# Kernel optimization log

Measured on AMD Instinct MI355X. Metric: run time of the kernel, lower is better.

## Reference

```python
import jax, jax.numpy as jnp
import numpy as np

# FCHL19 representation (Christensen et al., JCP 2020), as implemented by
# QMLightning's pairlist_gpu/egto_gpu/fchl_gpu CUDA kernels, re-expressed as
# dense masked pair/triplet tensors (non-periodic: cell/inv_cell empty).
SPECIES = np.array([1.0, 6.0, 7.0, 8.0], dtype=np.float32)
NSPEC = 4
NRS2 = 24
NRS3 = 20
RCUT = 8.0
ETA2 = 0.32
ETA3 = 2.7
TWO_BODY_DECAY = 1.8
THREE_BODY_DECAY = 0.57
THREE_BODY_WEIGHT = float(np.sqrt(ETA3 / np.pi) * 13.4)  # module pre-scales weight
RS2 = np.linspace(0.0, RCUT, NRS2 + 1)[1:].astype(np.float32)
RS3 = np.linspace(0.0, RCUT, NRS3 + 1)[1:].astype(np.float32)
NPAIR = NSPEC * (NSPEC + 1) // 2  # unordered species pairs -> 10

def _pair_map():
    M = np.zeros((NSPEC, NSPEC, NPAIR), np.float32)
    i = 0
    for p in range(NSPEC):
        for q in range(p, NSPEC):
            M[p, q, i] = 1.0
            M[q, p, i] = 1.0
            i += 1
    return M
PAIR_MAP = _pair_map()

B_MOL, MAX_ATOMS = 64, 28


def setup_inputs() -> dict:
    key = jax.random.key(0)
    k1, k2, k3 = jax.random.split(key, 3)
    X = jax.random.uniform(k1, (B_MOL, MAX_ATOMS, 3), jnp.float32) * 6.0
    atom_counts = jax.random.randint(k2, (B_MOL,), 24, MAX_ATOMS + 1).astype(jnp.int32)
    zidx = jax.random.randint(k3, (B_MOL, MAX_ATOMS), 0, NSPEC)
    valid = jnp.arange(MAX_ATOMS)[None, :] < atom_counts[:, None]
    Z = jnp.where(valid, jnp.asarray(SPECIES)[zidx], 0.0).astype(jnp.float32)
    atomIDs = jnp.arange(B_MOL * MAX_ATOMS, dtype=jnp.int32)
    molIDs = jnp.repeat(jnp.arange(B_MOL, dtype=jnp.int32), MAX_ATOMS)
    return {"X": X, "Z": Z, "atomIDs": atomIDs, "molIDs": molIDs, "atom_counts": atom_counts}


def _fchl(X, Z, atom_counts):
    B, N, _ = X.shape
    valid = jnp.arange(N)[None, :] < atom_counts[:, None]               # [B,N]
    diff = X[:, :, None, :] - X[:, None, :, :]                          # [B,N,N,3]
    d2 = jnp.sum(diff * diff, -1)
    eye = jnp.eye(N, dtype=bool)[None]
    pair_ok = valid[:, :, None] & valid[:, None, :] & (~eye)
    r = jnp.sqrt(jnp.where(pair_ok, d2, 1.0))                           # grad-safe distances
    within = pair_ok & (r < RCUT)
    fc = jnp.where(within, 0.5 * (jnp.cos(jnp.pi * r / RCUT) + 1.0), 0.0)
    oh = (Z[:, :, None] == jnp.asarray(SPECIES)[None, None, :]).astype(X.dtype)  # [B,N,S]

    # --- two-body: log-normal radial expansion, 1/r^decay scaling, cosine cutoff ---
    ln = jnp.log1p(ETA2 / (r * r))                                      # sigma^2
    mu = jnp.log(r) - 0.5 * ln
    rs2 = jnp.asarray(RS2)
    norm = 1.0 / (jnp.sqrt(ln)[..., None] * np.float32(np.sqrt(2.0 * np.pi)) * rs2)
    radial2 = (fc / jnp.power(r, TWO_BODY_DECAY))[..., None] * norm * \
        jnp.exp(-(jnp.log(rs2) - mu[..., None]) ** 2 / (2.0 * ln[..., None]))     # [B,N,N,M]
    rep2 = jnp.einsum('bijm,bjs->bism', radial2, oh).reshape(B, N, NSPEC * NRS2)

    # --- three-body: Axilrod-Teller-weighted radial x Fourier(order 1) angular ---
    rij = r[:, :, :, None]   # [B,i,j,1] -> broadcast over k
    rik = r[:, :, None, :]
    rjk = r[:, None, :, :]
    triu = (jnp.arange(N)[:, None] < jnp.arange(N)[None, :])[None, None]  # j<k
    m3 = within[:, :, :, None] & within[:, :, None, :] & triu
    rjk_s = jnp.where(m3, rjk, 1.0)
    cos_i = jnp.where(m3, (rij**2 + rik**2 - rjk_s**2) / (2.0 * rij * rik), 0.0)
    cos_j = (rij**2 + rjk_s**2 - rik**2) / (2.0 * rij * rjk_s)
    cos_k = (rik**2 + rjk_s**2 - rij**2) / (2.0 * rik * rjk_s)
    atm = (1.0 + 3.0 * cos_i * cos_j * cos_k) / jnp.power(rij * rik * rjk_s, THREE_BODY_DECAY)
    w = jnp.where(m3, THREE_BODY_WEIGHT * atm * fc[:, :, :, None] * fc[:, :, None, :], 0.0)
    c = jnp.clip(cos_i, -1.0, 1.0)
    s = jnp.sqrt(jnp.clip(1.0 - c * c, 1e-12, 1.0))
    ang = jnp.stack([2.0 * c, 2.0 * s], -1) * w[..., None]              # [B,N,N,N,2]
    radial3 = jnp.exp(-ETA3 * (0.5 * (rij + rik)[..., None] - jnp.asarray(RS3)) ** 2)  # [B,N,N,N,L]
    pair_oh = jnp.einsum('bjp,bkq,pqP->bjkP', oh, oh, jnp.asarray(PAIR_MAP))           # [B,N,N,10]
    t = jnp.einsum('bijka,bjkP->bijkaP', ang, pair_oh)
    rep3 = jnp.einsum('bijkaP,bijkl->biPla', t, radial3).reshape(B, N, NPAIR * NRS3 * 2)

    return jnp.concatenate([rep2, rep3], -1)  # [B,N,496]


def reference(X, Z, atomIDs, molIDs, atom_counts):
    # atomIDs/molIDs are CUDA block-assignment bookkeeping; math doesn't use them.
    return _fchl(X, Z, atom_counts)
```

## Files before the change

kernel.cpp:

```cpp
#include <hip/hip_runtime.h>

#define B_MOL 64
#define MAXN 28
#define NSPEC 4
#define NRS2 24
#define NRS3 20
#define NPAIR 10
#define NCOMB 378
#define REP2_LEN (NSPEC * NRS2)
#define REP3_LEN (NPAIR * NRS3 * 2)
#define OUT_LEN (REP2_LEN + REP3_LEN)
#define NTASK (NPAIR * NRS3 + REP2_LEN)
#define RCUT 8.0f
#define ETA2 0.32f
#define ETA3 2.7f
#define LOG2E 1.4426950408889634f
#define LN2F 0.6931471805599453f
#define W3 12.4225783348083f

__device__ __forceinline__ float hexp2(float x) { return __builtin_amdgcn_exp2f(x); }
__device__ __forceinline__ float hlog2(float x) { return __builtin_amdgcn_logf(x); }
__device__ __forceinline__ float hrcp(float x)  { return __builtin_amdgcn_rcpf(x); }
__device__ __forceinline__ float hrsq(float x)  { return __builtin_amdgcn_rsqf(x); }
__device__ __forceinline__ float hcos_rev(float t) { return __builtin_amdgcn_cosf(t); }

struct PairTab { unsigned short jk[NCOMB]; };
static constexpr PairTab make_tab() {
    PairTab t{};
    int idx = 0;
    for (int j = 0; j < MAXN; ++j)
        for (int k = j + 1; k < MAXN; ++k)
            t.jk[idx++] = (unsigned short)((j << 8) | k);
    return t;
}
__constant__ PairTab PT = make_tab();

__global__ __launch_bounds__(128) void fchl_kernel(
    const float* __restrict__ X,
    const float* __restrict__ Z,
    const int* __restrict__ counts,
    float* __restrict__ out)
{
    const int i = blockIdx.x;
    const int b = blockIdx.y;
    const int tid = threadIdx.x;
    const int cnt = counts[b];

    __shared__ float sx[MAXN], sy[MAXN], szc[MAXN];
    __shared__ int   s_win[MAXN];
    __shared__ float s_r[MAXN], s_fc[MAXN], s_mu[MAXN], s_i2ln[MAXN], s_pref[MAXN];
    __shared__ int   sspec[MAXN];
    __shared__ int   cntP[NPAIR], curP[NPAIR];
    __shared__ int   cntSp[NSPEC];
    __shared__ int   spList[NSPEC][MAXN];
    __shared__ float4 s_pair[NCOMB];

    float* orow = out + (size_t)(b * MAXN + i) * OUT_LEN;

    if (tid >= 28 && tid < 28 + NSPEC) cntSp[tid - 28] = 0;
    if (tid >= 64 && tid < 64 + NPAIR) { cntP[tid - 64] = 0; curP[tid - 64] = 0; }
    if (tid < MAXN) {
        const int j = tid;
        float xi = X[(b * MAXN + i) * 3 + 0];
        float yi = X[(b * MAXN + i) * 3 + 1];
        float zi = X[(b * MAXN + i) * 3 + 2];
        float xj = X[(b * MAXN + j) * 3 + 0];
        float yj = X[(b * MAXN + j) * 3 + 1];
        float zj = X[(b * MAXN + j) * 3 + 2];
        sx[j] = xj; sy[j] = yj; szc[j] = zj;
        float z = Z[b * MAXN + j];
        int s = -1;
        if (z == 1.0f) s = 0;
        else if (z == 6.0f) s = 1;
        else if (z == 7.0f) s = 2;
        else if (z == 8.0f) s = 3;
        sspec[j] = s;

        float dx = xi - xj, dy = yi - yj, dz = zi - zj;
        float r = sqrtf(dx * dx + dy * dy + dz * dz);
        bool w = (i < cnt) && (j < cnt) && (j != i) && (r < RCUT);
        s_win[j] = w ? 1 : 0;
        if (w) {
            float fc = 0.5f * (hcos_rev(r * (1.0f / 16.0f)) + 1.0f);
            float ln = LN2F * hlog2(1.0f + ETA2 * hrcp(r * r));
            float lr = LN2F * hlog2(r);
            s_r[j] = r;
            s_fc[j] = fc;
            s_mu[j] = lr - 0.5f * ln;
            s_i2ln[j] = LOG2E / (2.0f * ln);
            s_pref[j] = fc * hexp2(-1.8f * hlog2(r)) * hrsq(ln);
            int pos = atomicAdd(&cntSp[s], 1);
            spList[s][pos] = j;
        } else {
            s_r[j] = 1.0f; s_fc[j] = 0.0f; s_mu[j] = 0.0f;
            s_i2ln[j] = 1.0f; s_pref[j] = 0.0f;
        }
    }
    __syncthreads();

    float avgv[3], w0v[3], w1v[3];
    int   tagv[3];
    #pragma unroll
    for (int p = 0; p < 3; ++p) {
        int idx = tid + p * 128;
        int tg = -1; float av = 0.f, a0 = 0.f, a1 = 0.f;
        if (idx < NCOMB) {
            int jk = PT.jk[idx];
            int j = jk >> 8, k = jk & 255;
            if (s_win[j] && s_win[k]) {
                float rij = s_r[j], rik = s_r[k];
                float dx = sx[j] - sx[k], dy = sy[j] - sy[k], dz = szc[j] - szc[k];
                float rjk = sqrtf(dx * dx + dy * dy + dz * dz);

                float rij2 = rij * rij, rik2 = rik * rik, rjk2 = rjk * rjk;
                float cos_i = (rij2 + rik2 - rjk2) * 0.5f * hrcp(rij * rik);
                float cos_j = (rij2 + rjk2 - rik2) * 0.5f * hrcp(rij * rjk);
                float cos_k = (rik2 + rjk2 - rij2) * 0.5f * hrcp(rik * rjk);

                float atm = (1.0f + 3.0f * cos_i * cos_j * cos_k)
                            * hexp2(-0.57f * hlog2(rij * rik * rjk));
                float w = W3 * atm * s_fc[j] * s_fc[k];

                float c = fminf(fmaxf(cos_i, -1.0f), 1.0f);
                float sn = sqrtf(fminf(fmaxf(1.0f - c * c, 1e-12f), 1.0f));

                int pj = sspec[j], pk = sspec[k];
                int pp = min(pj, pk), q = max(pj, pk);
                tg = pp * NSPEC - (pp * (pp - 1)) / 2 + (q - pp);
                atomicAdd(&cntP[tg], 1);
                av = 0.5f * (rij + rik);
                a0 = 2.0f * c * w;
                a1 = 2.0f * sn * w;
            }
        }
        tagv[p] = tg; avgv[p] = av; w0v[p] = a0; w1v[p] = a1;
    }
    __syncthreads();

    #pragma unroll
    for (int p = 0; p < 3; ++p) {
        int tg = tagv[p];
        if (tg >= 0) {
            int bs = 0;
            #pragma unroll
            for (int q = 0; q < NPAIR - 1; ++q) bs += (q < tg) ? cntP[q] : 0;
            int slot = bs + atomicAdd(&curP[tg], 1);
            s_pair[slot] = make_float4(avgv[p], w0v[p], w1v[p], 0.0f);
        }
    }
    __syncthreads();

    for (int t = tid; t < NTASK; t += 128) {
        if (t < NPAIR * NRS3) {
            const int P = t / NRS3;
            const int l = t % NRS3;
            const float rs = 0.4f * (float)(l + 1);
            int s0 = 0;
            #pragma unroll
            for (int q = 0; q < NPAIR - 1; ++q) s0 += (q < P) ? cntP[q] : 0;
            const int s1 = s0 + cntP[P];
            float acc0 = 0.0f, acc1 = 0.0f;
            for (int s = s0; s < s1; ++s) {
                float4 pd = s_pair[s];
                float dd = pd.x - rs;
                float e = hexp2(-(ETA3 * LOG2E) * dd * dd);
                acc0 += pd.y * e;
                acc1 += pd.z * e;
            }
            orow[REP2_LEN + P * (NRS3 * 2) + l * 2 + 0] = acc0;
            orow[REP2_LEN + P * (NRS3 * 2) + l * 2 + 1] = acc1;
        } else {
            const int t2 = t - NPAIR * NRS3;
            const int sp = t2 / NRS2;
            const int m = t2 % NRS2;
            const float rs2 = (float)(m + 1) * (8.0f / 24.0f);
            const float lrs2 = LN2F * hlog2(rs2);
            const float nrm = 0.3989422804014327f / rs2;
            float acc = 0.0f;
            const int n = cntSp[sp];
            for (int c = 0; c < n; ++c) {
                int j = spList[sp][c];
                float d = lrs2 - s_mu[j];
                acc += s_pref[j] * hexp2(-d * d * s_i2ln[j]);
            }
            orow[sp * NRS2 + m] = acc * nrm;
        }
    }
}

extern "C" void kernel_launch(void* const* d_in, const int* in_sizes, int n_in,
                              void* d_out, int out_size, void* d_ws, size_t ws_size,
                              hipStream_t stream) {
    const float* X = (const float*)d_in[0];
    const float* Z = (const float*)d_in[1];
    const int* counts = (const int*)d_in[4];
    float* out = (float*)d_out;

    dim3 grid(MAXN, B_MOL);
    dim3 block(128);
    hipLaunchKernelGGL(fchl_kernel, grid, block, 0, stream, X, Z, counts, out);
}
```

Measured before the change: 20.76 us.

## Double block size to 256 threads and remap triplet and bin work

Raises the block size from 128 to 256 threads. Each thread now handles at most two triplet pairs instead of three, and the rep2 and rep3 bin tasks are spread across both halves of the block instead of a strided loop. It also software-prefetches the next s_pair entry in the bin accumulation loop. The aim is to shorten the serial per-thread chains in every phase, at the cost of more idle threads and a larger block per atom.

```diff
diff --git a/kernel.cpp b/kernel.cpp
--- a/kernel.cpp
+++ b/kernel.cpp
@@ -10,7 +10,7 @@
 #define REP2_LEN (NSPEC * NRS2)
 #define REP3_LEN (NPAIR * NRS3 * 2)
 #define OUT_LEN (REP2_LEN + REP3_LEN)
-#define NTASK (NPAIR * NRS3 + REP2_LEN)
+#define NBIN3 (NPAIR * NRS3)
 #define RCUT 8.0f
 #define ETA2 0.32f
 #define ETA3 2.7f
@@ -35,7 +35,7 @@
 }
 __constant__ PairTab PT = make_tab();
 
-__global__ __launch_bounds__(128) void fchl_kernel(
+__global__ __launch_bounds__(256) void fchl_kernel(
     const float* __restrict__ X,
     const float* __restrict__ Z,
     const int* __restrict__ counts,
@@ -98,81 +98,80 @@
     }
     __syncthreads();
 
-    float avgv[3], w0v[3], w1v[3];
-    int   tagv[3];
-    #pragma unroll
-    for (int p = 0; p < 3; ++p) {
-        int idx = tid + p * 128;
-        int tg = -1; float av = 0.f, a0 = 0.f, a1 = 0.f;
-        if (idx < NCOMB) {
-            int jk = PT.jk[idx];
-            int j = jk >> 8, k = jk & 255;
-            if (s_win[j] && s_win[k]) {
-                float rij = s_r[j], rik = s_r[k];
-                float dx = sx[j] - sx[k], dy = sy[j] - sy[k], dz = szc[j] - szc[k];
-                float rjk = sqrtf(dx * dx + dy * dy + dz * dz);
-
-                float rij2 = rij * rij, rik2 = rik * rik, rjk2 = rjk * rjk;
-                float cos_i = (rij2 + rik2 - rjk2) * 0.5f * hrcp(rij * rik);
-                float cos_j = (rij2 + rjk2 - rik2) * 0.5f * hrcp(rij * rjk);
-                float cos_k = (rik2 + rjk2 - rij2) * 0.5f * hrcp(rik * rjk);
-
-                float atm = (1.0f + 3.0f * cos_i * cos_j * cos_k)
-                            * hexp2(-0.57f * hlog2(rij * rik * rjk));
-                float w = W3 * atm * s_fc[j] * s_fc[k];
-
-                float c = fminf(fmaxf(cos_i, -1.0f), 1.0f);
-                float sn = sqrtf(fminf(fmaxf(1.0f - c * c, 1e-12f), 1.0f));
-
-                int pj = sspec[j], pk = sspec[k];
-                int pp = min(pj, pk), q = max(pj, pk);
-                tg = pp * NSPEC - (pp * (pp - 1)) / 2 + (q - pp);
-                atomicAdd(&cntP[tg], 1);
-                av = 0.5f * (rij + rik);
-                a0 = 2.0f * c * w;
-                a1 = 2.0f * sn * w;
-            }
-        }
-        tagv[p] = tg; avgv[p] = av; w0v[p] = a0; w1v[p] = a1;
+    float av0 = 0.f, a00 = 0.f, a10 = 0.f; int tg0 = -1;
+    float av1 = 0.f, a01 = 0.f, a11 = 0.f; int tg1 = -1;
+    {
+        int jk = PT.jk[tid];
+        int j = jk >> 8, k = jk & 255;
+        if (s_win[j] && s_win[k]) {
+            float rij = s_r[j], rik = s_r[k];
+            float dx = sx[j] - sx[k], dy = sy[j] - sy[k], dz = szc[j] - szc[k];
+            float rjk = sqrtf(dx * dx + dy * dy + dz * dz);
+            float rij2 = rij * rij, rik2 = rik * rik, rjk2 = rjk * rjk;
+            float cos_i = (rij2 + rik2 - rjk2) * 0.5f * hrcp(rij * rik);
+            float cos_j = (rij2 + rjk2 - rik2) * 0.5f * hrcp(rij * rjk);
+            float cos_k = (rik2 + rjk2 - rij2) * 0.5f * hrcp(rik * rjk);
+            float atm = (1.0f + 3.0f * cos_i * cos_j * cos_k)
+                        * hexp2(-0.57f * hlog2(rij * rik * rjk));
+            float w = W3 * atm * s_fc[j] * s_fc[k];
+            float c = fminf(fmaxf(cos_i, -1.0f), 1.0f);
+            float sn = sqrtf(fminf(fmaxf(1.0f - c * c, 1e-12f), 1.0f));
+            int pj = sspec[j], pk = sspec[k];
+            int pp = min(pj, pk), q = max(pj, pk);
+            tg0 = pp * NSPEC - (pp * (pp - 1)) / 2 + (q - pp);
+            atomicAdd(&cntP[tg0], 1);
+            av0 = 0.5f * (rij + rik);
+            a00 = 2.0f * c * w;
+            a10 = 2.0f * sn * w;
+        }
+    }
+    if (tid < NCOMB - 256) {
+        int jk = PT.jk[tid + 256];
+        int j = jk >> 8, k = jk & 255;
+        if (s_win[j] && s_win[k]) {
+            float rij = s_r[j], rik = s_r[k];
+            float dx = sx[j] - sx[k], dy = sy[j] - sy[k], dz = szc[j] - szc[k];
+            float rjk = sqrtf(dx * dx + dy * dy + dz * dz);
+            float rij2 = rij * rij, rik2 = rik * rik, rjk2 = rjk * rjk;
+            float cos_i = (rij2 + rik2 - rjk2) * 0.5f * hrcp(rij * rik);
+            float cos_j = (rij2 + rjk2 - rik2) * 0.5f * hrcp(rij * rjk);
+            float cos_k = (rik2 + rjk2 - rij2) * 0.5f * hrcp(rik * rjk);
+            float atm = (1.0f + 3.0f * cos_i * cos_j * cos_k)
+                        * hexp2(-0.57f * hlog2(rij * rik * rjk));
+            float w = W3 * atm * s_fc[j] * s_fc[k];
+            float c = fminf(fmaxf(cos_i, -1.0f), 1.0f);
+            float sn = sqrtf(fminf(fmaxf(1.0f - c * c, 1e-12f), 1.0f));
+            int pj = sspec[j], pk = sspec[k];
+            int pp = min(pj, pk), q = max(pj, pk);
+            tg1 = pp * NSPEC - (pp * (pp - 1)) / 2 + (q - pp);
+            atomicAdd(&cntP[tg1], 1);
+            av1 = 0.5f * (rij + rik);
+            a01 = 2.0f * c * w;
+            a11 = 2.0f * sn * w;
+        }
     }
     __syncthreads();
 
-    #pragma unroll
-    for (int p = 0; p < 3; ++p) {
-        int tg = tagv[p];
-        if (tg >= 0) {
-            int bs = 0;
-            #pragma unroll
-            for (int q = 0; q < NPAIR - 1; ++q) bs += (q < tg) ? cntP[q] : 0;
-            int slot = bs + atomicAdd(&curP[tg], 1);
-            s_pair[slot] = make_float4(avgv[p], w0v[p], w1v[p], 0.0f);
-        }
+    if (tg0 >= 0) {
+        int bs = 0;
+        #pragma unroll
+        for (int q = 0; q < NPAIR - 1; ++q) bs += (q < tg0) ? cntP[q] : 0;
+        int slot = bs + atomicAdd(&curP[tg0], 1);
+        s_pair[slot] = make_float4(av0, a00, a10, 0.0f);
+    }
+    if (tg1 >= 0) {
+        int bs = 0;
+        #pragma unroll
+        for (int q = 0; q < NPAIR - 1; ++q) bs += (q < tg1) ? cntP[q] : 0;
+        int slot = bs + atomicAdd(&curP[tg1], 1);
+        s_pair[slot] = make_float4(av1, a01, a11, 0.0f);
     }
     __syncthreads();
 
-    for (int t = tid; t < NTASK; t += 128) {
-        if (t < NPAIR * NRS3) {
-            const int P = t / NRS3;
-            const int l = t % NRS3;
-            const float rs = 0.4f * (float)(l + 1);
-            int s0 = 0;
-            #pragma unroll
-            for (int q = 0; q < NPAIR - 1; ++q) s0 += (q < P) ? cntP[q] : 0;
-            const int s1 = s0 + cntP[P];
-            float acc0 = 0.0f, acc1 = 0.0f;
-            for (int s = s0; s < s1; ++s) {
-                float4 pd = s_pair[s];
-                float dd = pd.x - rs;
-                float e = hexp2(-(ETA3 * LOG2E) * dd * dd);
-                acc0 += pd.y * e;
-                acc1 += pd.z * e;
-            }
-            orow[REP2_LEN + P * (NRS3 * 2) + l * 2 + 0] = acc0;
-            orow[REP2_LEN + P * (NRS3 * 2) + l * 2 + 1] = acc1;
-        } else {
-            const int t2 = t - NPAIR * NRS3;
-            const int sp = t2 / NRS2;
-            const int m = t2 % NRS2;
+    if (tid < 128) {
+        if (tid < REP2_LEN) {
+            const int sp = tid / NRS2;
+            const int m = tid % NRS2;
             const float rs2 = (float)(m + 1) * (8.0f / 24.0f);
             const float lrs2 = LN2F * hlog2(rs2);
             const float nrm = 0.3989422804014327f / rs2;
@@ -185,6 +184,49 @@
             }
             orow[sp * NRS2 + m] = acc * nrm;
         }
+    } else {
+        const int g = tid - 128;
+        const int P = g / NRS3;
+        const int l = g % NRS3;
+        const float rs = 0.4f * (float)(l + 1);
+        int s0 = 0;
+        #pragma unroll
+        for (int q = 0; q < NPAIR - 1; ++q) s0 += (q < P) ? cntP[q] : 0;
+        const int s1 = s0 + cntP[P];
+        float acc0 = 0.0f, acc1 = 0.0f;
+        float4 pd = (s0 < s1) ? s_pair[s0] : make_float4(0.f, 0.f, 0.f, 0.f);
+        for (int s = s0; s < s1; ++s) {
+            float4 nx = (s + 1 < s1) ? s_pair[s + 1] : pd;
+            float dd = pd.x - rs;
+            float e = hexp2(-(ETA3 * LOG2E) * dd * dd);
+            acc0 += pd.y * e;
+            acc1 += pd.z * e;
+            pd = nx;
+        }
+        orow[REP2_LEN + P * (NRS3 * 2) + l * 2 + 0] = acc0;
+        orow[REP2_LEN + P * (NRS3 * 2) + l * 2 + 1] = acc1;
+    }
+    if (tid < NBIN3 - 128) {
+        const int g = 128 + tid;
+        const int P = g / NRS3;
+        const int l = g % NRS3;
+        const float rs = 0.4f * (float)(l + 1);
+        int s0 = 0;
+        #pragma unroll
+        for (int q = 0; q < NPAIR - 1; ++q) s0 += (q < P) ? cntP[q] : 0;
+        const int s1 = s0 + cntP[P];
+        float acc0 = 0.0f, acc1 = 0.0f;
+        float4 pd = (s0 < s1) ? s_pair[s0] : make_float4(0.f, 0.f, 0.f, 0.f);
+        for (int s = s0; s < s1; ++s) {
+            float4 nx = (s + 1 < s1) ? s_pair[s + 1] : pd;
+            float dd = pd.x - rs;
+            float e = hexp2(-(ETA3 * LOG2E) * dd * dd);
+            acc0 += pd.y * e;
+            acc1 += pd.z * e;
+            pd = nx;
+        }
+        orow[REP2_LEN + P * (NRS3 * 2) + l * 2 + 0] = acc0;
+        orow[REP2_LEN + P * (NRS3 * 2) + l * 2 + 1] = acc1;
     }
 }
 
@@ -197,6 +239,6 @@
     float* out = (float*)d_out;
 
     dim3 grid(MAXN, B_MOL);
-    dim3 block(128);
+    dim3 block(256);
     hipLaunchKernelGGL(fchl_kernel, grid, block, 0, stream, X, Z, counts, out);
 }
```

Result: slower. 48.42 us (+133.2%).
